# Optimization experiments

Hardware: AMD Instinct MI355X
Metric: run time of the kernel (lower is better)

The kernel has to match this reference:

```python
import jax, jax.numpy as jnp
import numpy as np

G, D, F, B, T = 8, 20, 160, 64, 2000  # groups, dims(hidden), feature=G*D, batch, time


def _lstm_layer(x, Wih, Whh, bih, bhh):
    # x: [B, T, Din]; Wih: [4H, Din]; Whh: [4H, H]; PyTorch gate order i,f,g,o
    H = Whh.shape[1]
    xw = jnp.einsum('btd,gd->btg', x, Wih) + bih + bhh  # [B, T, 4H]
    xw = jnp.swapaxes(xw, 0, 1)  # [T, B, 4H]
    h0 = jnp.zeros((x.shape[0], H), x.dtype)

    def step(carry, xw_t):
        h, c = carry
        gates = xw_t + h @ Whh.T
        i, f, g, o = jnp.split(gates, 4, axis=-1)
        c = jax.nn.sigmoid(f) * c + jax.nn.sigmoid(i) * jnp.tanh(g)
        h = jax.nn.sigmoid(o) * jnp.tanh(c)
        return (h, c), h

    _, hs = jax.lax.scan(step, (h0, h0), xw)
    return jnp.swapaxes(hs, 0, 1)  # [B, T, H]


def _lstm2(xg, Wih0, Whh0, bih0, bhh0, Wih1, Whh1, bih1, bhh1):
    h = _lstm_layer(xg, Wih0, Whh0, bih0, bhh0)
    return _lstm_layer(h, Wih1, Whh1, bih1, bhh1)


_run_groups = jax.vmap(_lstm2)  # map over leading group axis of inputs and params


def setup_inputs() -> dict:
    key = jax.random.key(0)
    ks = jax.random.split(key, 14)
    s = 1.0 / np.sqrt(D)
    inp = {
        'x': jax.random.normal(ks[0], (B, T, G, D), jnp.float32),
        'W_ih0': jax.random.uniform(ks[1], (G, 4 * D, D), jnp.float32, -s, s),
        'W_hh0': jax.random.uniform(ks[2], (G, 4 * D, D), jnp.float32, -s, s),
        'b_ih0': jax.random.uniform(ks[3], (G, 4 * D), jnp.float32, -s, s),
        'b_hh0': jax.random.uniform(ks[4], (G, 4 * D), jnp.float32, -s, s),
        'W_ih1': jax.random.uniform(ks[5], (G, 4 * D, D), jnp.float32, -s, s),
        'W_hh1': jax.random.uniform(ks[6], (G, 4 * D, D), jnp.float32, -s, s),
        'b_ih1': jax.random.uniform(ks[7], (G, 4 * D), jnp.float32, -s, s),
        'b_hh1': jax.random.uniform(ks[8], (G, 4 * D), jnp.float32, -s, s),
        'W1': jax.random.uniform(ks[9], (4 * F, F), jnp.float32, -1 / np.sqrt(F), 1 / np.sqrt(F)),
        'b1': jax.random.uniform(ks[10], (4 * F,), jnp.float32, -1 / np.sqrt(F), 1 / np.sqrt(F)),
        'W2': jax.random.uniform(ks[11], (F, 4 * F), jnp.float32, -1 / np.sqrt(4 * F), 1 / np.sqrt(4 * F)),
        'b2': jax.random.uniform(ks[12], (F,), jnp.float32, -1 / np.sqrt(4 * F), 1 / np.sqrt(4 * F)),
    }
    return inp


def reference(x, W_ih0, W_hh0, b_ih0, b_hh0, W_ih1, W_hh1, b_ih1, b_hh1, W1, b1, W2, b2):
    # x: [B, T, G, D] -> per-group 2-layer LSTM -> concat bands -> residual -> MLP
    xg = jnp.transpose(x, (2, 0, 1, 3))  # [G, B, T, D]
    out = _run_groups(xg, W_ih0, W_hh0, b_ih0, b_hh0, W_ih1, W_hh1, b_ih1, b_hh1)  # [G, B, T, D]
    out = jnp.transpose(out, (1, 2, 0, 3)).reshape(x.shape[0], x.shape[1], G * D)  # [B, T, F]
    fullband = out + x.reshape(x.shape[0], x.shape[1], G * D)
    h = jax.nn.relu(fullband @ W1.T + b1)
    return h @ W2.T + b2  # [B, T, F]
```

## Files before the change

### kernel.cpp

```cpp
#include <hip/hip_runtime.h>


#define Gn 8
#define Dn 20
#define Bn 64
#define Tn 2000
#define Fn 160
#define NR (Bn * Tn)
#define L2E 1.4426950408889634f
#define WS_W1 0
#define WS_W2 102400
#define WS_NEED (204800 * sizeof(unsigned short))

typedef __attribute__((ext_vector_type(2))) float f32x2;
typedef __attribute__((ext_vector_type(4))) float f32x4;
typedef __attribute__((ext_vector_type(8))) short bf16x8;
typedef __attribute__((ext_vector_type(2))) unsigned u32x2;

__device__ __forceinline__ float rdlane(float v, int k) {
  return __int_as_float(__builtin_amdgcn_readlane(__float_as_int(v), k));
}
__device__ __forceinline__ float xswap(float v) {
#if __has_builtin(__builtin_amdgcn_permlane32_swap)
  const u32x2 r = __builtin_amdgcn_permlane32_swap(__float_as_uint(v),
                                                   __float_as_uint(v), false,
                                                   false);
  return __uint_as_float(r.y);
#else
  return __shfl_xor(v, 32);
#endif
}
__device__ __forceinline__ unsigned short f2bf(float f) {
  unsigned u = __float_as_uint(f);
  u += 0x8000u;
  return (unsigned short)(u >> 16);
}

__device__ __forceinline__ void rec2(float gzA, float gzB,
                                     const f32x2* __restrict__ WPA,
                                     const f32x2* __restrict__ WPB, float& h,
                                     float& c) {
  f32x2 hp[10];
#pragma unroll
  for (int j = 0; j < 10; ++j) {
    hp[j].x = rdlane(h, 2 * j);
    hp[j].y = rdlane(h, 2 * j + 1);
  }
  f32x2 aA0, aA1, aB0, aB1;
  aA0.x = gzA; aA0.y = 0.f;
  aA1.x = 0.f; aA1.y = 0.f;
  aB0.x = gzB; aB0.y = 0.f;
  aB1.x = 0.f; aB1.y = 0.f;
#pragma unroll
  for (int j = 0; j < 10; j += 2) {
    aA0 = __builtin_elementwise_fma(WPA[j], hp[j], aA0);
    aA1 = __builtin_elementwise_fma(WPA[j + 1], hp[j + 1], aA1);
    aB0 = __builtin_elementwise_fma(WPB[j], hp[j], aB0);
    aB1 = __builtin_elementwise_fma(WPB[j + 1], hp[j + 1], aB1);
  }
  const float zA = (aA0.x + aA0.y) + (aA1.x + aA1.y);
  const float zB = (aB0.x + aB0.y) + (aB1.x + aB1.y);
  const float rA = __builtin_amdgcn_rcpf(1.f + __builtin_amdgcn_exp2f(zA));
  const float rB = __builtin_amdgcn_rcpf(1.f + __builtin_amdgcn_exp2f(zB));
  const float sF = xswap(rA);
  const float sO = xswap(rB);
  const float tG = __builtin_fmaf(-2.f, rB, 1.f);
  c = sF * c + rA * tG;
  const float tC = __builtin_fmaf(
      -2.f, __builtin_amdgcn_rcpf(1.f + __builtin_amdgcn_exp2f((2.f * L2E) * c)),
      1.f);
  h = sO * tC;
}

__device__ __forceinline__ void proj2(const float* __restrict__ row,
                                      const f32x2* __restrict__ WPA,
                                      const f32x2* __restrict__ WPB, float bzA,
                                      float bzB, float* dA, float* dB) {
  const f32x4 x0 = *(const f32x4*)&row[0];
  const f32x4 x1 = *(const f32x4*)&row[4];
  const f32x4 x2 = *(const f32x4*)&row[8];
  const f32x4 x3 = *(const f32x4*)&row[12];
  const f32x4 x4 = *(const f32x4*)&row[16];
  f32x2 xp[10];
  xp[0] = __builtin_shufflevector(x0, x0, 0, 1);
  xp[1] = __builtin_shufflevector(x0, x0, 2, 3);
  xp[2] = __builtin_shufflevector(x1, x1, 0, 1);
  xp[3] = __builtin_shufflevector(x1, x1, 2, 3);
  xp[4] = __builtin_shufflevector(x2, x2, 0, 1);
  xp[5] = __builtin_shufflevector(x2, x2, 2, 3);
  xp[6] = __builtin_shufflevector(x3, x3, 0, 1);
  xp[7] = __builtin_shufflevector(x3, x3, 2, 3);
  xp[8] = __builtin_shufflevector(x4, x4, 0, 1);
  xp[9] = __builtin_shufflevector(x4, x4, 2, 3);
  f32x2 aA0, aA1, aB0, aB1;
  aA0.x = bzA; aA0.y = 0.f;
  aA1.x = 0.f; aA1.y = 0.f;
  aB0.x = bzB; aB0.y = 0.f;
  aB1.x = 0.f; aB1.y = 0.f;
#pragma unroll
  for (int j = 0; j < 10; j += 2) {
    aA0 = __builtin_elementwise_fma(WPA[j], xp[j], aA0);
    aA1 = __builtin_elementwise_fma(WPA[j + 1], xp[j + 1], aA1);
    aB0 = __builtin_elementwise_fma(WPB[j], xp[j], aB0);
    aB1 = __builtin_elementwise_fma(WPB[j + 1], xp[j + 1], aB1);
  }
  *dA = (aA0.x + aA0.y) + (aA1.x + aA1.y);
  *dB = (aB0.x + aB0.y) + (aB1.x + aB1.y);
}

__global__ __launch_bounds__(512) void scan4p_kernel(
    const float* __restrict__ x, const float* __restrict__ Wih0,
    const float* __restrict__ Whh0, const float* __restrict__ bih0,
    const float* __restrict__ bhh0, const float* __restrict__ Wih1,
    const float* __restrict__ Whh1, const float* __restrict__ bih1,
    const float* __restrict__ bhh1, float* __restrict__ out) {
  __shared__ __align__(16) float XS[2][64][20];
  __shared__ __align__(16) float XW0[2][16][128];
  __shared__ __align__(16) float XW1[2][16][128];
  __shared__ __align__(16) float H0[2][16][20];

  const int tid = threadIdx.x;
  const int lane = tid & 63;
  const int wv = tid >> 6;
  const int sub = wv >> 2;
  const int wr = wv & 3;
  const int role = sub ? (3 - wr) : wr;
  const int chain = blockIdx.x * 2 + sub;
  const int g = chain >> 6;
  const int b = chain & 63;

  float (*const xs)[20] = XS[sub];
  float (*const xw0)[128] = XW0[sub];
  float (*const xw1)[128] = XW1[sub];
  float (*const h0r)[20] = H0[sub];

  const bool wl = lane < Dn;

  int rowA, rowB;
  float sAc, sBc;
  if (lane < 20) {
    rowA = lane; rowB = lane + 40; sAc = -L2E; sBc = 2.f * L2E;
  } else if (lane >= 32 && lane < 52) {
    rowA = lane - 12; rowB = lane + 28; sAc = -L2E; sBc = -L2E;
  } else {
    rowA = 0; rowB = 0; sAc = 0.f; sBc = 0.f;
  }

  f32x2 WPA[10], WPB[10];
  float bzA = 0.f, bzB = 0.f;
  {
    const float* Wsrc;
    const float* bi = nullptr;
    const float* bh = nullptr;
    if (role == 0) {
      Wsrc = Wih0; bi = bih0; bh = bhh0;
    } else if (role == 1) {
      Wsrc = Whh0;
    } else if (role == 2) {
      Wsrc = Wih1; bi = bih1; bh = bhh1;
    } else {
      Wsrc = Whh1;
    }
    const float* Wg = Wsrc + g * 1600;
#pragma unroll
    for (int j = 0; j < 10; ++j) {
      WPA[j].x = Wg[rowA * 20 + 2 * j] * sAc;
      WPA[j].y = Wg[rowA * 20 + 2 * j + 1] * sAc;
      WPB[j].x = Wg[rowB * 20 + 2 * j] * sBc;
      WPB[j].y = Wg[rowB * 20 + 2 * j + 1] * sBc;
    }
    if (bi) {
      bzA = (bi[g * 80 + rowA] + bh[g * 80 + rowA]) * sAc;
      bzB = (bi[g * 80 + rowB] + bh[g * 80 + rowB]) * sBc;
    }
  }

  if (role & 1) __builtin_amdgcn_s_setprio(1);

  const long long cbase = (long long)b * (Tn * Fn) + g * Dn;

  int st_t[3], st_d[3];
  bool st_v[3];
#pragma unroll
  for (int i = 0; i < 3; ++i) {
    const int idx = lane + 64 * i;
    st_v[i] = idx < 160;
    st_t[i] = idx / 20;
    st_d[i] = idx % 20;
  }

  if (role == 0) {
#pragma unroll
    for (int i = 0; i < 3; ++i)
      if (st_v[i])
        xs[st_t[i]][st_d[i]] = x[cbase + (long long)st_t[i] * Fn + st_d[i]];
  }
  __syncthreads();

  float h = 0.f, c = 0.f;

  for (int cix = 0; cix <= 252; ++cix) {
    if (role == 0) {
      const int cs = cix + 1;
      const bool dostage = (cs <= 249);
      float sv[3];
      if (dostage) {
#pragma unroll
        for (int i = 0; i < 3; ++i)
          if (st_v[i])
            sv[i] = x[cbase + (long long)(cs * 8 + st_t[i]) * Fn + st_d[i]];
      }
      if (cix <= 249) {
        const float* xsp = &xs[(cix * 8) & 63][0];
        float* xwp = &xw0[(cix * 8) & 15][0];
#pragma unroll
        for (int p = 0; p < 8; ++p)
          proj2(&xsp[p * 20], WPA, WPB, bzA, bzB, &xwp[p * 128 + lane],
                &xwp[p * 128 + 64 + lane]);
      }
      if (dostage) {
        float* xsw = &xs[(cs * 8) & 63][0];
#pragma unroll
        for (int i = 0; i < 3; ++i)
          if (st_v[i]) xsw[st_t[i] * 20 + st_d[i]] = sv[i];
      }
    } else if (role == 1) {
      if (cix >= 1 && cix <= 250) {
        const float* xwp = &xw0[((cix - 1) * 8) & 15][0];
        float* hrw = &h0r[((cix - 1) * 8) & 15][0];
        float gzA[8], gzB[8];
#pragma unroll
        for (int p = 0; p < 8; ++p) {
          gzA[p] = xwp[p * 128 + lane];
          gzB[p] = xwp[p * 128 + 64 + lane];
        }
#pragma unroll
        for (int p = 0; p < 8; ++p) {
          rec2(gzA[p], gzB[p], WPA, WPB, h, c);
          if (wl) hrw[p * 20 + lane] = h;
        }
      }
    } else if (role == 2) {
      if (cix >= 2 && cix <= 251) {
        const float* hrp = &h0r[((cix - 2) * 8) & 15][0];
        float* xwp = &xw1[((cix - 2) * 8) & 15][0];
#pragma unroll
        for (int p = 0; p < 8; ++p)
          proj2(&hrp[p * 20], WPA, WPB, bzA, bzB, &xwp[p * 128 + lane],
                &xwp[p * 128 + 64 + lane]);
      }
    } else {
      if (cix >= 3) {
        const int c8 = (cix - 3) * 8;
        const int rl = wl ? lane : 0;
        const float* xwp = &xw1[c8 & 15][0];
        const float* xsp = &xs[c8 & 63][0];
        float gzA[8], gzB[8], xr[8];
#pragma unroll
        for (int p = 0; p < 8; ++p) {
          gzA[p] = xwp[p * 128 + lane];
          gzB[p] = xwp[p * 128 + 64 + lane];
          xr[p] = xsp[p * 20 + rl];
        }
#pragma unroll
        for (int p = 0; p < 8; ++p) {
          rec2(gzA[p], gzB[p], WPA, WPB, h, c);
          if (wl) out[cbase + (long long)(c8 + p) * Fn + lane] = h + xr[p];
        }
      }
    }
    __syncthreads();
  }
}

__global__ __launch_bounds__(256) void wprep_kernel(
    const float* __restrict__ W1, const float* __restrict__ W2,
    unsigned short* __restrict__ wb) {
  const int t = blockIdx.x * 256 + threadIdx.x;
  const float4 v = (t < 25600) ? *(const float4*)(W1 + t * 4)
                               : *(const float4*)(W2 + (t - 25600) * 4);
  *(ushort4*)(wb + t * 4) =
      make_ushort4(f2bf(v.x), f2bf(v.y), f2bf(v.z), f2bf(v.w));
}

__global__ __launch_bounds__(256) void mlp_bf16w_kernel(
    float* io, const unsigned short* __restrict__ wb,
    const float* __restrict__ b1, const float* __restrict__ b2) {
  __shared__ short Ab[64 * 168];
  __shared__ short Wb[64 * 168];
  __shared__ short Hb[64 * 72];
  __shared__ short W2b[160 * 72];
  const unsigned short* __restrict__ W1b = wb + WS_W1;
  const unsigned short* __restrict__ W2s = wb + WS_W2;
  const int tid = threadIdx.x;
  const int lane = tid & 63;
  const int wv = tid >> 6;
  const long long r0 = (long long)blockIdx.x * 64;

#pragma unroll
  for (int i = 0; i < 10; ++i) {
    const int idx = tid + i * 256;
    const int r = idx / 40, kq = idx % 40;
    const float4 v = *(const float4*)(io + (r0 + r) * Fn + kq * 4);
    *(ushort4*)&Ab[r * 168 + kq * 4] =
        make_ushort4(f2bf(v.x), f2bf(v.y), f2bf(v.z), f2bf(v.w));
  }
  __syncthreads();

  const int cl = lane & 15;
  const int q8 = (lane >> 4) * 8;
  const int ar = wv * 16 + cl;
  bf16x8 afr[5];
#pragma unroll
  for (int kk = 0; kk < 5; ++kk)
    afr[kk] = *(const bf16x8*)&Ab[ar * 168 + kk * 32 + q8];

  f32x4 acc[10];
#pragma unroll
  for (int n = 0; n < 10; ++n) acc[n] = (f32x4){0.f, 0.f, 0.f, 0.f};

  for (int nc = 0; nc < 10; ++nc) {
    if (nc) __syncthreads();
#pragma unroll
    for (int i = 0; i < 10; ++i) {
      const int idx = tid + i * 256;
      const int r = idx / 40, kq = idx % 40;
      *(ushort4*)&Wb[r * 168 + kq * 4] =
          *(const ushort4*)(W1b + (nc * 64 + r) * 160 + kq * 4);
    }
#pragma unroll
    for (int i = 0; i < 10; ++i) {
      const int idx = tid + i * 256;
      const int n = idx >> 4, kq = idx & 15;
      *(ushort4*)&W2b[n * 72 + kq * 4] =
          *(const ushort4*)(W2s + n * 640 + nc * 64 + kq * 4);
    }
    __syncthreads();
#pragma unroll
    for (int n16 = 0; n16 < 4; ++n16) {
      f32x4 hcc = (f32x4){0.f, 0.f, 0.f, 0.f};
      const int br = n16 * 16 + cl;
#pragma unroll
      for (int kk = 0; kk < 5; ++kk) {
        const bf16x8 bfr = *(const bf16x8*)&Wb[br * 168 + kk * 32 + q8];
        hcc = __builtin_amdgcn_mfma_f32_16x16x32_bf16(afr[kk], bfr, hcc, 0, 0, 0);
      }
      const float b1v = b1[nc * 64 + n16 * 16 + cl];
      const int hrow0 = wv * 16 + (lane >> 4) * 4;
      const int hcol = n16 * 16 + cl;
#pragma unroll
      for (int r = 0; r < 4; ++r)
        Hb[(hrow0 + r) * 72 + hcol] = f2bf(fmaxf(hcc[r] + b1v, 0.f));
    }
    bf16x8 a2[2];
#pragma unroll
    for (int kk = 0; kk < 2; ++kk)
      a2[kk] = *(const bf16x8*)&Hb[ar * 72 + kk * 32 + q8];
#pragma unroll
    for (int n16 = 0; n16 < 10; ++n16) {
      const int br = n16 * 16 + cl;
#pragma unroll
      for (int kk = 0; kk < 2; ++kk) {
        const bf16x8 b2f = *(const bf16x8*)&W2b[br * 72 + kk * 32 + q8];
        acc[n16] = __builtin_amdgcn_mfma_f32_16x16x32_bf16(a2[kk], b2f, acc[n16], 0, 0, 0);
      }
    }
  }
  const int orow0 = wv * 16 + (lane >> 4) * 4;
#pragma unroll
  for (int n16 = 0; n16 < 10; ++n16) {
    const float b2v = b2[n16 * 16 + cl];
#pragma unroll
    for (int r = 0; r < 4; ++r)
      io[(r0 + orow0 + r) * Fn + n16 * 16 + cl] = acc[n16][r] + b2v;
  }
}

__global__ __launch_bounds__(256) void mlp_mfma_kernel(
    float* io, const float* __restrict__ W1, const float* __restrict__ b1,
    const float* __restrict__ W2, const float* __restrict__ b2) {
  __shared__ short Ab[64 * 168];
  __shared__ short Wb[64 * 168];
  __shared__ short Hb[64 * 72];
  __shared__ short W2b[160 * 72];
  const int tid = threadIdx.x;
  const int lane = tid & 63;
  const int wv = tid >> 6;
  const long long r0 = (long long)blockIdx.x * 64;

#pragma unroll
  for (int i = 0; i < 10; ++i) {
    const int idx = tid + i * 256;
    const int r = idx / 40, kq = idx % 40;
    const float4 v = *(const float4*)(io + (r0 + r) * Fn + kq * 4);
    *(ushort4*)&Ab[r * 168 + kq * 4] =
        make_ushort4(f2bf(v.x), f2bf(v.y), f2bf(v.z), f2bf(v.w));
  }
  __syncthreads();

  const int cl = lane & 15;
  const int q8 = (lane >> 4) * 8;
  const int ar = wv * 16 + cl;
  bf16x8 afr[5];
#pragma unroll
  for (int kk = 0; kk < 5; ++kk)
    afr[kk] = *(const bf16x8*)&Ab[ar * 168 + kk * 32 + q8];

  f32x4 acc[10];
#pragma unroll
  for (int n = 0; n < 10; ++n) acc[n] = (f32x4){0.f, 0.f, 0.f, 0.f};

  for (int nc = 0; nc < 10; ++nc) {
    if (nc) __syncthreads();
#pragma unroll
    for (int i = 0; i < 10; ++i) {
      const int idx = tid + i * 256;
      const int r = idx / 40, kq = idx % 40;
      const float4 v = *(const float4*)(W1 + (nc * 64 + r) * Fn + kq * 4);
      *(ushort4*)&Wb[r * 168 + kq * 4] =
          make_ushort4(f2bf(v.x), f2bf(v.y), f2bf(v.z), f2bf(v.w));
    }
#pragma unroll
    for (int i = 0; i < 10; ++i) {
      const int idx = tid + i * 256;
      const int n = idx >> 4, kq = idx & 15;
      const float4 v = *(const float4*)(W2 + n * 640 + nc * 64 + kq * 4);
      *(ushort4*)&W2b[n * 72 + kq * 4] =
          make_ushort4(f2bf(v.x), f2bf(v.y), f2bf(v.z), f2bf(v.w));
    }
    __syncthreads();
#pragma unroll
    for (int n16 = 0; n16 < 4; ++n16) {
      f32x4 hcc = (f32x4){0.f, 0.f, 0.f, 0.f};
      const int br = n16 * 16 + cl;
#pragma unroll
      for (int kk = 0; kk < 5; ++kk) {
        const bf16x8 bfr = *(const bf16x8*)&Wb[br * 168 + kk * 32 + q8];
        hcc = __builtin_amdgcn_mfma_f32_16x16x32_bf16(afr[kk], bfr, hcc, 0, 0, 0);
      }
      const float b1v = b1[nc * 64 + n16 * 16 + cl];
      const int hrow0 = wv * 16 + (lane >> 4) * 4;
      const int hcol = n16 * 16 + cl;
#pragma unroll
      for (int r = 0; r < 4; ++r)
        Hb[(hrow0 + r) * 72 + hcol] = f2bf(fmaxf(hcc[r] + b1v, 0.f));
    }
    bf16x8 a2[2];
#pragma unroll
    for (int kk = 0; kk < 2; ++kk)
      a2[kk] = *(const bf16x8*)&Hb[ar * 72 + kk * 32 + q8];
#pragma unroll
    for (int n16 = 0; n16 < 10; ++n16) {
      const int br = n16 * 16 + cl;
#pragma unroll
      for (int kk = 0; kk < 2; ++kk) {
        const bf16x8 b2f = *(const bf16x8*)&W2b[br * 72 + kk * 32 + q8];
        acc[n16] = __builtin_amdgcn_mfma_f32_16x16x32_bf16(a2[kk], b2f, acc[n16], 0, 0, 0);
      }
    }
  }
  const int orow0 = wv * 16 + (lane >> 4) * 4;
#pragma unroll
  for (int n16 = 0; n16 < 10; ++n16) {
    const float b2v = b2[n16 * 16 + cl];
#pragma unroll
    for (int r = 0; r < 4; ++r)
      io[(r0 + orow0 + r) * Fn + n16 * 16 + cl] = acc[n16][r] + b2v;
  }
}

extern "C" void kernel_launch(void* const* d_in, const int* in_sizes, int n_in,
                              void* d_out, int out_size, void* d_ws, size_t ws_size,
                              hipStream_t stream) {
  const float* x    = (const float*)d_in[0];
  const float* Wih0 = (const float*)d_in[1];
  const float* Whh0 = (const float*)d_in[2];
  const float* bih0 = (const float*)d_in[3];
  const float* bhh0 = (const float*)d_in[4];
  const float* Wih1 = (const float*)d_in[5];
  const float* Whh1 = (const float*)d_in[6];
  const float* bih1 = (const float*)d_in[7];
  const float* bhh1 = (const float*)d_in[8];
  const float* W1   = (const float*)d_in[9];
  const float* b1   = (const float*)d_in[10];
  const float* W2   = (const float*)d_in[11];
  const float* b2   = (const float*)d_in[12];
  float* out = (float*)d_out;

  const bool fast = (d_ws != nullptr) && (ws_size >= WS_NEED);
  if (fast)
    wprep_kernel<<<dim3(200), dim3(256), 0, stream>>>(
        W1, W2, (unsigned short*)d_ws);

  scan4p_kernel<<<dim3(256), dim3(512), 0, stream>>>(
      x, Wih0, Whh0, bih0, bhh0, Wih1, Whh1, bih1, bhh1, out);

  if (fast)
    mlp_bf16w_kernel<<<dim3(NR / 64), dim3(256), 0, stream>>>(
        out, (const unsigned short*)d_ws, b1, b2);
  else
    mlp_mfma_kernel<<<dim3(NR / 64), dim3(256), 0, stream>>>(out, W1, b1, W2, b2);
}
```

Before: 729.6 us.

## Prefetch next MLP weight chunk into registers during MFMA compute

```diff
diff --git a/kernel.cpp b/kernel.cpp
--- a/kernel.cpp
+++ b/kernel.cpp
@@ -46,20 +46,19 @@
     hp[j].x = rdlane(h, 2 * j);
     hp[j].y = rdlane(h, 2 * j + 1);
   }
-  f32x2 aA0, aA1, aB0, aB1;
-  aA0.x = gzA; aA0.y = 0.f;
-  aA1.x = 0.f; aA1.y = 0.f;
-  aB0.x = gzB; aB0.y = 0.f;
-  aB1.x = 0.f; aB1.y = 0.f;
-#pragma unroll
-  for (int j = 0; j < 10; j += 2) {
-    aA0 = __builtin_elementwise_fma(WPA[j], hp[j], aA0);
-    aA1 = __builtin_elementwise_fma(WPA[j + 1], hp[j + 1], aA1);
-    aB0 = __builtin_elementwise_fma(WPB[j], hp[j], aB0);
-    aB1 = __builtin_elementwise_fma(WPB[j + 1], hp[j + 1], aB1);
-  }
-  const float zA = (aA0.x + aA0.y) + (aA1.x + aA1.y);
-  const float zB = (aB0.x + aB0.y) + (aB1.x + aB1.y);
+  f32x2 aA;
+  aA.x = gzA;
+  aA.y = 0.f;
+  f32x2 aB;
+  aB.x = gzB;
+  aB.y = 0.f;
+#pragma unroll
+  for (int j = 0; j < 10; ++j) {
+    aA = __builtin_elementwise_fma(WPA[j], hp[j], aA);
+    aB = __builtin_elementwise_fma(WPB[j], hp[j], aB);
+  }
+  const float zA = aA.x + aA.y;
+  const float zB = aB.x + aB.y;
   const float rA = __builtin_amdgcn_rcpf(1.f + __builtin_amdgcn_exp2f(zA));
   const float rB = __builtin_amdgcn_rcpf(1.f + __builtin_amdgcn_exp2f(zB));
   const float sF = xswap(rA);
@@ -92,20 +91,19 @@
   xp[7] = __builtin_shufflevector(x3, x3, 2, 3);
   xp[8] = __builtin_shufflevector(x4, x4, 0, 1);
   xp[9] = __builtin_shufflevector(x4, x4, 2, 3);
-  f32x2 aA0, aA1, aB0, aB1;
-  aA0.x = bzA; aA0.y = 0.f;
-  aA1.x = 0.f; aA1.y = 0.f;
-  aB0.x = bzB; aB0.y = 0.f;
-  aB1.x = 0.f; aB1.y = 0.f;
-#pragma unroll
-  for (int j = 0; j < 10; j += 2) {
-    aA0 = __builtin_elementwise_fma(WPA[j], xp[j], aA0);
-    aA1 = __builtin_elementwise_fma(WPA[j + 1], xp[j + 1], aA1);
-    aB0 = __builtin_elementwise_fma(WPB[j], xp[j], aB0);
-    aB1 = __builtin_elementwise_fma(WPB[j + 1], xp[j + 1], aB1);
-  }
-  *dA = (aA0.x + aA0.y) + (aA1.x + aA1.y);
-  *dB = (aB0.x + aB0.y) + (aB1.x + aB1.y);
+  f32x2 aA;
+  aA.x = bzA;
+  aA.y = 0.f;
+  f32x2 aB;
+  aB.x = bzB;
+  aB.y = 0.f;
+#pragma unroll
+  for (int j = 0; j < 10; ++j) {
+    aA = __builtin_elementwise_fma(WPA[j], xp[j], aA);
+    aB = __builtin_elementwise_fma(WPB[j], xp[j], aB);
+  }
+  *dA = aA.x + aA.y;
+  *dB = aB.x + aB.y;
 }
 
 __global__ __launch_bounds__(512) void scan4p_kernel(
@@ -283,6 +281,42 @@
       make_ushort4(f2bf(v.x), f2bf(v.y), f2bf(v.z), f2bf(v.w));
 }
 
+__device__ __forceinline__ void mlp_compute(
+    const short* __restrict__ Wb, const short* __restrict__ W2b,
+    short* __restrict__ Hb, const bf16x8* afr, f32x4* acc,
+    const float* __restrict__ b1, int nc, int wv, int lane, int cl, int q8,
+    int ar) {
+#pragma unroll
+  for (int n16 = 0; n16 < 4; ++n16) {
+    f32x4 hcc = (f32x4){0.f, 0.f, 0.f, 0.f};
+    const int br = n16 * 16 + cl;
+#pragma unroll
+    for (int kk = 0; kk < 5; ++kk) {
+      const bf16x8 bfr = *(const bf16x8*)&Wb[br * 168 + kk * 32 + q8];
+      hcc = __builtin_amdgcn_mfma_f32_16x16x32_bf16(afr[kk], bfr, hcc, 0, 0, 0);
+    }
+    const float b1v = b1[nc * 64 + n16 * 16 + cl];
+    const int hrow0 = wv * 16 + (lane >> 4) * 4;
+    const int hcol = n16 * 16 + cl;
+#pragma unroll
+    for (int r = 0; r < 4; ++r)
+      Hb[(hrow0 + r) * 72 + hcol] = f2bf(fmaxf(hcc[r] + b1v, 0.f));
+  }
+  bf16x8 a2[2];
+#pragma unroll
+  for (int kk = 0; kk < 2; ++kk)
+    a2[kk] = *(const bf16x8*)&Hb[ar * 72 + kk * 32 + q8];
+#pragma unroll
+  for (int n16 = 0; n16 < 10; ++n16) {
+    const int br = n16 * 16 + cl;
+#pragma unroll
+    for (int kk = 0; kk < 2; ++kk) {
+      const bf16x8 b2f = *(const bf16x8*)&W2b[br * 72 + kk * 32 + q8];
+      acc[n16] = __builtin_amdgcn_mfma_f32_16x16x32_bf16(a2[kk], b2f, acc[n16], 0, 0, 0);
+    }
+  }
+}
+
 __global__ __launch_bounds__(256) void mlp_bf16w_kernel(
     float* io, const unsigned short* __restrict__ wb,
     const float* __restrict__ b1, const float* __restrict__ b2) {
@@ -297,6 +331,13 @@
   const int wv = tid >> 6;
   const long long r0 = (long long)blockIdx.x * 64;
 
+  ushort4 wa1[10], wa2[10], wn1[10], wn2[10];
+#pragma unroll
+  for (int i = 0; i < 10; ++i) {
+    const int idx = tid + i * 256;
+    wa1[i] = *(const ushort4*)(W1b + (idx / 40) * 160 + (idx % 40) * 4);
+    wa2[i] = *(const ushort4*)(W2s + (idx >> 4) * 640 + (idx & 15) * 4);
+  }
 #pragma unroll
   for (int i = 0; i < 10; ++i) {
     const int idx = tid + i * 256;
@@ -319,52 +360,41 @@
 #pragma unroll
   for (int n = 0; n < 10; ++n) acc[n] = (f32x4){0.f, 0.f, 0.f, 0.f};
 
-  for (int nc = 0; nc < 10; ++nc) {
-    if (nc) __syncthreads();
+#pragma unroll
+  for (int ncp = 0; ncp < 5; ++ncp) {
+    const int nc0 = 2 * ncp, nc1 = 2 * ncp + 1;
+    if (nc0) __syncthreads();
 #pragma unroll
     for (int i = 0; i < 10; ++i) {
       const int idx = tid + i * 256;
-      const int r = idx / 40, kq = idx % 40;
-      *(ushort4*)&Wb[r * 168 + kq * 4] =
-          *(const ushort4*)(W1b + (nc * 64 + r) * 160 + kq * 4);
+      *(ushort4*)&Wb[(idx / 40) * 168 + (idx % 40) * 4] = wa1[i];
+      *(ushort4*)&W2b[(idx >> 4) * 72 + (idx & 15) * 4] = wa2[i];
     }
 #pragma unroll
     for (int i = 0; i < 10; ++i) {
       const int idx = tid + i * 256;
-      const int n = idx >> 4, kq = idx & 15;
-      *(ushort4*)&W2b[n * 72 + kq * 4] =
-          *(const ushort4*)(W2s + n * 640 + nc * 64 + kq * 4);
+      wn1[i] = *(const ushort4*)(W1b + (nc1 * 64 + idx / 40) * 160 + (idx % 40) * 4);
+      wn2[i] = *(const ushort4*)(W2s + (idx >> 4) * 640 + nc1 * 64 + (idx & 15) * 4);
     }
     __syncthreads();
-#pragma unroll
-    for (int n16 = 0; n16 < 4; ++n16) {
-      f32x4 hcc = (f32x4){0.f, 0.f, 0.f, 0.f};
-      const int br = n16 * 16 + cl;
-#pragma unroll
-      for (int kk = 0; kk < 5; ++kk) {
-        const bf16x8 bfr = *(const bf16x8*)&Wb[br * 168 + kk * 32 + q8];
-        hcc = __builtin_amdgcn_mfma_f32_16x16x32_bf16(afr[kk], bfr, hcc, 0, 0, 0);
-      }
-      const float b1v = b1[nc * 64 + n16 * 16 + cl];
-      const int hrow0 = wv * 16 + (lane >> 4) * 4;
-      const int hcol = n16 * 16 + cl;
-#pragma unroll
-      for (int r = 0; r < 4; ++r)
-        Hb[(hrow0 + r) * 72 + hcol] = f2bf(fmaxf(hcc[r] + b1v, 0.f));
-    }
-    bf16x8 a2[2];
-#pragma unroll
-    for (int kk = 0; kk < 2; ++kk)
-      a2[kk] = *(const bf16x8*)&Hb[ar * 72 + kk * 32 + q8];
-#pragma unroll
-    for (int n16 = 0; n16 < 10; ++n16) {
-      const int br = n16 * 16 + cl;
-#pragma unroll
-      for (int kk = 0; kk < 2; ++kk) {
-        const bf16x8 b2f = *(const bf16x8*)&W2b[br * 72 + kk * 32 + q8];
-        acc[n16] = __builtin_amdgcn_mfma_f32_16x16x32_bf16(a2[kk], b2f, acc[n16], 0, 0, 0);
-      }
-    }
+    mlp_compute(Wb, W2b, Hb, afr, acc, b1, nc0, wv, lane, cl, q8, ar);
+    __syncthreads();
+#pragma unroll
+    for (int i = 0; i < 10; ++i) {
+      const int idx = tid + i * 256;
+      *(ushort4*)&Wb[(idx / 40) * 168 + (idx % 40) * 4] = wn1[i];
+      *(ushort4*)&W2b[(idx >> 4) * 72 + (idx & 15) * 4] = wn2[i];
+    }
+    if (ncp < 4) {
+#pragma unroll
+      for (int i = 0; i < 10; ++i) {
+        const int idx = tid + i * 256;
+        wa1[i] = *(const ushort4*)(W1b + ((nc1 + 1) * 64 + idx / 40) * 160 + (idx % 40) * 4);
+        wa2[i] = *(const ushort4*)(W2s + (idx >> 4) * 640 + (nc1 + 1) * 64 + (idx & 15) * 4);
+      }
+    }
+    __syncthreads();
+    mlp_compute(Wb, W2b, Hb, afr, acc, b1, nc1, wv, lane, cl, q8, ar);
   }
   const int orow0 = wv * 16 + (lane >> 4) * 4;
 #pragma unroll
@@ -429,35 +459,7 @@
           make_ushort4(f2bf(v.x), f2bf(v.y), f2bf(v.z), f2bf(v.w));
     }
     __syncthreads();
-#pragma unroll
-    for (int n16 = 0; n16 < 4; ++n16) {
-      f32x4 hcc = (f32x4){0.f, 0.f, 0.f, 0.f};
-      const int br = n16 * 16 + cl;
-#pragma unroll
-      for (int kk = 0; kk < 5; ++kk) {
-        const bf16x8 bfr = *(const bf16x8*)&Wb[br * 168 + kk * 32 + q8];
-        hcc = __builtin_amdgcn_mfma_f32_16x16x32_bf16(afr[kk], bfr, hcc, 0, 0, 0);
-      }
-      const float b1v = b1[nc * 64 + n16 * 16 + cl];
-      const int hrow0 = wv * 16 + (lane >> 4) * 4;
-      const int hcol = n16 * 16 + cl;
-#pragma unroll
-      for (int r = 0; r < 4; ++r)
-        Hb[(hrow0 + r) * 72 + hcol] = f2bf(fmaxf(hcc[r] + b1v, 0.f));
-    }
-    bf16x8 a2[2];
-#pragma unroll
-    for (int kk = 0; kk < 2; ++kk)
-      a2[kk] = *(const bf16x8*)&Hb[ar * 72 + kk * 32 + q8];
-#pragma unroll
-    for (int n16 = 0; n16 < 10; ++n16) {
-      const int br = n16 * 16 + cl;
-#pragma unroll
-      for (int kk = 0; kk < 2; ++kk) {
-        const bf16x8 b2f = *(const bf16x8*)&W2b[br * 72 + kk * 32 + q8];
-        acc[n16] = __builtin_amdgcn_mfma_f32_16x16x32_bf16(a2[kk], b2f, acc[n16], 0, 0, 0);
-      }
-    }
+    mlp_compute(Wb, W2b, Hb, afr, acc, b1, nc, wv, lane, cl, q8, ar);
   }
   const int orow0 = wv * 16 + (lane >> 4) * 4;
 #pragma unroll
```

New measurement: 694.8 us. 1.05x faster.

## Double pipeline chunk size to 16 steps and use single-chain FMA accumulation

Applied to the files above, without the earlier changes.

```diff
diff --git a/kernel.cpp b/kernel.cpp
--- a/kernel.cpp
+++ b/kernel.cpp
@@ -46,20 +46,19 @@
     hp[j].x = rdlane(h, 2 * j);
     hp[j].y = rdlane(h, 2 * j + 1);
   }
-  f32x2 aA0, aA1, aB0, aB1;
-  aA0.x = gzA; aA0.y = 0.f;
-  aA1.x = 0.f; aA1.y = 0.f;
-  aB0.x = gzB; aB0.y = 0.f;
-  aB1.x = 0.f; aB1.y = 0.f;
-#pragma unroll
-  for (int j = 0; j < 10; j += 2) {
-    aA0 = __builtin_elementwise_fma(WPA[j], hp[j], aA0);
-    aA1 = __builtin_elementwise_fma(WPA[j + 1], hp[j + 1], aA1);
-    aB0 = __builtin_elementwise_fma(WPB[j], hp[j], aB0);
-    aB1 = __builtin_elementwise_fma(WPB[j + 1], hp[j + 1], aB1);
-  }
-  const float zA = (aA0.x + aA0.y) + (aA1.x + aA1.y);
-  const float zB = (aB0.x + aB0.y) + (aB1.x + aB1.y);
+  f32x2 aA;
+  aA.x = gzA;
+  aA.y = 0.f;
+  f32x2 aB;
+  aB.x = gzB;
+  aB.y = 0.f;
+#pragma unroll
+  for (int j = 0; j < 10; ++j) {
+    aA = __builtin_elementwise_fma(WPA[j], hp[j], aA);
+    aB = __builtin_elementwise_fma(WPB[j], hp[j], aB);
+  }
+  const float zA = aA.x + aA.y;
+  const float zB = aB.x + aB.y;
   const float rA = __builtin_amdgcn_rcpf(1.f + __builtin_amdgcn_exp2f(zA));
   const float rB = __builtin_amdgcn_rcpf(1.f + __builtin_amdgcn_exp2f(zB));
   const float sF = xswap(rA);
@@ -92,20 +91,19 @@
   xp[7] = __builtin_shufflevector(x3, x3, 2, 3);
   xp[8] = __builtin_shufflevector(x4, x4, 0, 1);
   xp[9] = __builtin_shufflevector(x4, x4, 2, 3);
-  f32x2 aA0, aA1, aB0, aB1;
-  aA0.x = bzA; aA0.y = 0.f;
-  aA1.x = 0.f; aA1.y = 0.f;
-  aB0.x = bzB; aB0.y = 0.f;
-  aB1.x = 0.f; aB1.y = 0.f;
-#pragma unroll
-  for (int j = 0; j < 10; j += 2) {
-    aA0 = __builtin_elementwise_fma(WPA[j], xp[j], aA0);
-    aA1 = __builtin_elementwise_fma(WPA[j + 1], xp[j + 1], aA1);
-    aB0 = __builtin_elementwise_fma(WPB[j], xp[j], aB0);
-    aB1 = __builtin_elementwise_fma(WPB[j + 1], xp[j + 1], aB1);
-  }
-  *dA = (aA0.x + aA0.y) + (aA1.x + aA1.y);
-  *dB = (aB0.x + aB0.y) + (aB1.x + aB1.y);
+  f32x2 aA;
+  aA.x = bzA;
+  aA.y = 0.f;
+  f32x2 aB;
+  aB.x = bzB;
+  aB.y = 0.f;
+#pragma unroll
+  for (int j = 0; j < 10; ++j) {
+    aA = __builtin_elementwise_fma(WPA[j], xp[j], aA);
+    aB = __builtin_elementwise_fma(WPB[j], xp[j], aB);
+  }
+  *dA = aA.x + aA.y;
+  *dB = aB.x + aB.y;
 }
 
 __global__ __launch_bounds__(512) void scan4p_kernel(
@@ -114,10 +112,10 @@
     const float* __restrict__ bhh0, const float* __restrict__ Wih1,
     const float* __restrict__ Whh1, const float* __restrict__ bih1,
     const float* __restrict__ bhh1, float* __restrict__ out) {
-  __shared__ __align__(16) float XS[2][64][20];
-  __shared__ __align__(16) float XW0[2][16][128];
-  __shared__ __align__(16) float XW1[2][16][128];
-  __shared__ __align__(16) float H0[2][16][20];
+  __shared__ __align__(16) float XS[2][128][20];
+  __shared__ __align__(16) float XW0[2][32][128];
+  __shared__ __align__(16) float XW1[2][32][128];
+  __shared__ __align__(16) float H0[2][32][20];
 
   const int tid = threadIdx.x;
   const int lane = tid & 63;
@@ -179,93 +177,88 @@
 
   const long long cbase = (long long)b * (Tn * Fn) + g * Dn;
 
-  int st_t[3], st_d[3];
-  bool st_v[3];
-#pragma unroll
-  for (int i = 0; i < 3; ++i) {
+  int st_t[5], st_d[5];
+#pragma unroll
+  for (int i = 0; i < 5; ++i) {
     const int idx = lane + 64 * i;
-    st_v[i] = idx < 160;
     st_t[i] = idx / 20;
     st_d[i] = idx % 20;
   }
 
   if (role == 0) {
 #pragma unroll
-    for (int i = 0; i < 3; ++i)
-      if (st_v[i])
-        xs[st_t[i]][st_d[i]] = x[cbase + (long long)st_t[i] * Fn + st_d[i]];
+    for (int i = 0; i < 5; ++i)
+      xs[st_t[i]][st_d[i]] = x[cbase + (long long)st_t[i] * Fn + st_d[i]];
   }
   __syncthreads();
 
   float h = 0.f, c = 0.f;
 
-  for (int cix = 0; cix <= 252; ++cix) {
+  for (int cix = 0; cix <= 127; ++cix) {
     if (role == 0) {
       const int cs = cix + 1;
-      const bool dostage = (cs <= 249);
-      float sv[3];
+      const bool dostage = (cs <= 124);
+      float sv[5];
       if (dostage) {
 #pragma unroll
-        for (int i = 0; i < 3; ++i)
-          if (st_v[i])
-            sv[i] = x[cbase + (long long)(cs * 8 + st_t[i]) * Fn + st_d[i]];
-      }
-      if (cix <= 249) {
-        const float* xsp = &xs[(cix * 8) & 63][0];
-        float* xwp = &xw0[(cix * 8) & 15][0];
-#pragma unroll
-        for (int p = 0; p < 8; ++p)
+        for (int i = 0; i < 5; ++i)
+          sv[i] = x[cbase + (long long)(cs * 16 + st_t[i]) * Fn + st_d[i]];
+      }
+      if (cix <= 124) {
+        const float* xsp = &xs[(cix * 16) & 127][0];
+        float* xwp = &xw0[(cix * 16) & 31][0];
+#pragma unroll
+        for (int p = 0; p < 16; ++p)
           proj2(&xsp[p * 20], WPA, WPB, bzA, bzB, &xwp[p * 128 + lane],
                 &xwp[p * 128 + 64 + lane]);
       }
       if (dostage) {
-        float* xsw = &xs[(cs * 8) & 63][0];
-#pragma unroll
-        for (int i = 0; i < 3; ++i)
-          if (st_v[i]) xsw[st_t[i] * 20 + st_d[i]] = sv[i];
+        float* xsw = &xs[(cs * 16) & 127][0];
+#pragma unroll
+        for (int i = 0; i < 5; ++i) xsw[st_t[i] * 20 + st_d[i]] = sv[i];
       }
     } else if (role == 1) {
-      if (cix >= 1 && cix <= 250) {
-        const float* xwp = &xw0[((cix - 1) * 8) & 15][0];
-        float* hrw = &h0r[((cix - 1) * 8) & 15][0];
-        float gzA[8], gzB[8];
-#pragma unroll
-        for (int p = 0; p < 8; ++p) {
+      if (cix >= 1 && cix <= 125) {
+        const float* xwp = &xw0[((cix - 1) * 16) & 31][0];
+        float* hrw = &h0r[((cix - 1) * 16) & 31][0];
+        float gzA[16], gzB[16];
+#pragma unroll
+        for (int p = 0; p < 16; ++p) {
           gzA[p] = xwp[p * 128 + lane];
           gzB[p] = xwp[p * 128 + 64 + lane];
         }
 #pragma unroll
-        for (int p = 0; p < 8; ++p) {
+        for (int p = 0; p < 16; ++p) {
           rec2(gzA[p], gzB[p], WPA, WPB, h, c);
           if (wl) hrw[p * 20 + lane] = h;
         }
       }
     } else if (role == 2) {
-      if (cix >= 2 && cix <= 251) {
-        const float* hrp = &h0r[((cix - 2) * 8) & 15][0];
-        float* xwp = &xw1[((cix - 2) * 8) & 15][0];
-#pragma unroll
-        for (int p = 0; p < 8; ++p)
+      if (cix >= 2 && cix <= 126) {
+        const float* hrp = &h0r[((cix - 2) * 16) & 31][0];
+        float* xwp = &xw1[((cix - 2) * 16) & 31][0];
+#pragma unroll
+        for (int p = 0; p < 16; ++p)
           proj2(&hrp[p * 20], WPA, WPB, bzA, bzB, &xwp[p * 128 + lane],
                 &xwp[p * 128 + 64 + lane]);
       }
     } else {
       if (cix >= 3) {
-        const int c8 = (cix - 3) * 8;
+        const int c16 = (cix - 3) * 16;
         const int rl = wl ? lane : 0;
-        const float* xwp = &xw1[c8 & 15][0];
-        const float* xsp = &xs[c8 & 63][0];
-        float gzA[8], gzB[8], xr[8];
-#pragma unroll
-        for (int p = 0; p < 8; ++p) {
+        const float* xwp = &xw1[c16 & 31][0];
+        const float* xsp = &xs[c16 & 127][0];
+        float gzA[16], gzB[16], xr[16];
+#pragma unroll
+        for (int p = 0; p < 16; ++p) {
           gzA[p] = xwp[p * 128 + lane];
           gzB[p] = xwp[p * 128 + 64 + lane];
           xr[p] = xsp[p * 20 + rl];
         }
 #pragma unroll
-        for (int p = 0; p < 8; ++p) {
+        for (int p = 0; p < 16; ++p) {
           rec2(gzA[p], gzB[p], WPA, WPB, h, c);
-          if (wl) out[cbase + (long long)(c8 + p) * Fn + lane] = h + xr[p];
+          if (wl) out[cbase + (long long)(c16 + p) * Fn + lane] = h + xr[p];
         }
       }
     }
```

Result: faster. 670.4 us (-8.1%).
